# Optimization experiments

Measured on AMD Instinct MI355X. Metric: run time of the kernel, lower is better.

The kernel has to match this reference:

```python
import jax, jax.numpy as jnp
import numpy as np

N_NODES = 50000
N_EDGES = 1600000
D_IN = 128
D_OUT = 128
EPS = 0.001  # GINConv(eps=0.001) hard-coded in the module


def setup_inputs() -> dict:
    key = jax.random.key(0)
    k_x, k_e, k_w1, k_b1, k_w2, k_b2 = jax.random.split(key, 6)
    x = jax.random.normal(k_x, (N_NODES, D_IN), dtype=jnp.float32)
    edge_index = jax.random.randint(k_e, (2, N_EDGES), 0, N_NODES, dtype=jnp.int64)
    # MLP params (nn.Linear default init scale ~ 1/sqrt(fan_in))
    s1 = 1.0 / np.sqrt(D_IN)
    s2 = 1.0 / np.sqrt(D_OUT)
    W1 = jax.random.uniform(k_w1, (D_IN, D_OUT), jnp.float32, -s1, s1)
    b1 = jax.random.uniform(k_b1, (D_OUT,), jnp.float32, -s1, s1)
    W2 = jax.random.uniform(k_w2, (D_OUT, D_OUT), jnp.float32, -s2, s2)
    b2 = jax.random.uniform(k_b2, (D_OUT,), jnp.float32, -s2, s2)
    return {"x": x, "edge_index": edge_index, "W1": W1, "b1": b1, "W2": W2, "b2": b2}


def reference(x, edge_index, W1, b1, W2, b2):
    # GIN: out = MLP((1 + eps) * x + sum_{j in N(i)} x_j)
    src = edge_index[0]  # message source nodes
    dst = edge_index[1]  # aggregation targets
    agg = jax.ops.segment_sum(x[src], dst, num_segments=x.shape[0])  # [N, D_IN]
    h = (1.0 + EPS) * x + agg
    h = jax.nn.relu(h @ W1 + b1)
    return h @ W2 + b2
```

## Files before the change

### kernel.cpp

```cpp
#include <hip/hip_runtime.h>
#include <hip/hip_bf16.h>


#define N_NODES 50000
#define N_EDGES 1600000
#define D 128

#define NB_H 256
#define CHUNK (N_EDGES / NB_H)
#define EPT 7
#define BSH 6
#define BSZ 64
#define KB 782
#define CAPB 2560

typedef __attribute__((ext_vector_type(8))) short short8;
typedef __attribute__((ext_vector_type(4))) float float4v;

__device__ inline unsigned short f2b(float f) {
    unsigned u = __builtin_bit_cast(unsigned, f);
    u = u + 0x7fffu + ((u >> 16) & 1u);
    return (unsigned short)(u >> 16);
}
__device__ inline float b2f_lo(unsigned u) { return __builtin_bit_cast(float, u << 16); }
__device__ inline float b2f_hi(unsigned u) { return __builtin_bit_cast(float, u & 0xffff0000u); }

#define LPAD 136

__global__ __launch_bounds__(1024) void k_prep(const float* __restrict__ W1,
                                               const float* __restrict__ W2,
                                               unsigned short* __restrict__ Wt1,
                                               unsigned short* __restrict__ Wt2,
                                               unsigned* __restrict__ bpos,
                                               const int* __restrict__ ei,
                                               int* __restrict__ flag) {
    __shared__ int nz;
    if (threadIdx.x == 0) nz = 0;
    __syncthreads();
    if (blockIdx.x == 0 && threadIdx.x < 256 && ei[threadIdx.x * 2 + 1] != 0)
        atomicAdd(&nz, 1);
    __syncthreads();
    if (blockIdx.x == 0 && threadIdx.x == 0) *flag = (nz == 0) ? 1 : 0;
    if (blockIdx.x == 0)
        for (int i = threadIdx.x; i < KB; i += 1024) bpos[i] = 0u;

    const float* W = (blockIdx.x == 0) ? W1 : W2;
    unsigned short* Wt = (blockIdx.x == 0) ? Wt1 : Wt2;
    for (int i = threadIdx.x; i < 128 * 128; i += 1024) {
        int k = i >> 7;
        int n = i & 127;
        Wt[n * 128 + k] = f2b(W[k * 128 + n]);
    }
}

template <int AF32, int BIAS, int OUT_BF16>
__global__ __launch_bounds__(256, 2) void k_mm(const void* __restrict__ Av,
                                               const unsigned short* __restrict__ Wtg,
                                               const float* __restrict__ bias,
                                               void* __restrict__ outv, int M) {
    __shared__ short Al[128 * LPAD];
    __shared__ short Wt[128 * LPAD];
    __shared__ float bl[128];

    int t = threadIdx.x;
    int row0 = blockIdx.x * 128;

    if (AF32) {
        const float4* X4 = (const float4*)Av;
        #pragma unroll
        for (int i = 0; i < 16; ++i) {
            int idx = i * 256 + t;
            int r = idx >> 5;
            int c = idx & 31;
            float4 v = make_float4(0.f, 0.f, 0.f, 0.f);
            if (row0 + r < M) v = X4[(size_t)(row0 + r) * 32 + c];
            short4 o;
            o.x = (short)f2b(v.x); o.y = (short)f2b(v.y);
            o.z = (short)f2b(v.z); o.w = (short)f2b(v.w);
            *(short4*)&Al[r * LPAD + c * 4] = o;
        }
    } else {
        const uint4* A16 = (const uint4*)Av;
        #pragma unroll
        for (int i = 0; i < 8; ++i) {
            int idx = i * 256 + t;
            int r = idx >> 4;
            int c = idx & 15;
            uint4 v = make_uint4(0u, 0u, 0u, 0u);
            if (row0 + r < M) v = A16[(size_t)(row0 + r) * 16 + c];
            *(uint4*)&Al[r * LPAD + c * 8] = v;
        }
    }
    {
        const uint4* Wg4 = (const uint4*)Wtg;
        #pragma unroll
        for (int i = 0; i < 8; ++i) {
            int idx = i * 256 + t;
            int r = idx >> 4;
            int c = idx & 15;
            *(uint4*)&Wt[r * LPAD + c * 8] = Wg4[idx];
        }
    }
    if (BIAS && t < 32) ((float4*)bl)[t] = ((const float4*)bias)[t];
    __syncthreads();

    int wave = t >> 6;
    int lane = t & 63;
    int quad = lane >> 4;
    int l16 = lane & 15;
    int rowbase = wave * 32;

    float4v acc[2][8];
    #pragma unroll
    for (int mt = 0; mt < 2; ++mt)
        #pragma unroll
        for (int nt = 0; nt < 8; ++nt)
            acc[mt][nt] = (float4v){0.f, 0.f, 0.f, 0.f};

    #pragma unroll
    for (int kc = 0; kc < 4; ++kc) {
        int koff = kc * 32 + quad * 8;
        short8 a0 = *(const short8*)&Al[(rowbase + l16) * LPAD + koff];
        short8 a1 = *(const short8*)&Al[(rowbase + 16 + l16) * LPAD + koff];
        #pragma unroll
        for (int nt = 0; nt < 8; ++nt) {
            short8 bfr = *(const short8*)&Wt[(nt * 16 + l16) * LPAD + koff];
            acc[0][nt] = __builtin_amdgcn_mfma_f32_16x16x32_bf16(a0, bfr, acc[0][nt], 0, 0, 0);
            acc[1][nt] = __builtin_amdgcn_mfma_f32_16x16x32_bf16(a1, bfr, acc[1][nt], 0, 0, 0);
        }
    }

    #pragma unroll
    for (int mt = 0; mt < 2; ++mt) {
        int rloc = rowbase + mt * 16 + quad * 4;
        #pragma unroll
        for (int nt = 0; nt < 8; ++nt) {
            int col = nt * 16 + l16;
            float bv = BIAS ? bl[col] : 0.f;
            #pragma unroll
            for (int r = 0; r < 4; ++r) {
                int grow = row0 + rloc + r;
                if (grow < M) {
                    float v = acc[mt][nt][r] + bv;
                    if (OUT_BF16)
                        ((unsigned short*)outv)[(size_t)grow * 128 + col] = f2b(v);
                    else
                        ((float*)outv)[(size_t)grow * 128 + col] = v;
                }
            }
        }
    }
}

__global__ __launch_bounds__(1024) void k_sort(const int* __restrict__ ei,
                                               const int* __restrict__ flag,
                                               unsigned* __restrict__ bpos,
                                               unsigned* __restrict__ pairs) {
    __shared__ unsigned hist[KB];
    __shared__ unsigned bbase[KB];
    int b = blockIdx.x;
    int t = threadIdx.x;
    for (int i = t; i < KB; i += 1024) hist[i] = 0u;
    __syncthreads();
    int wide = *flag;
    int e0 = b * CHUNK;
    int dv[EPT], sv[EPT];
    #pragma unroll
    for (int i = 0; i < EPT; ++i) {
        dv[i] = -1; sv[i] = 0;
        int o = i * 1024 + t;
        if (o < CHUNK) {
            int e = e0 + o;
            long long di = (long long)N_EDGES + e;
            int d = wide ? ei[di * 2] : ei[di];
            int s = wide ? ei[(long long)e * 2] : ei[e];
            if ((unsigned)d < (unsigned)N_NODES) {
                dv[i] = d;
                sv[i] = ((unsigned)s < (unsigned)N_NODES) ? s : 0;
                atomicAdd(&hist[d >> BSH], 1u);
            }
        }
    }
    __syncthreads();
    for (int i = t; i < KB; i += 1024) {
        unsigned c = hist[i];
        bbase[i] = c ? atomicAdd(&bpos[i], c) : 0u;
        hist[i] = 0u;
    }
    __syncthreads();
    #pragma unroll
    for (int i = 0; i < EPT; ++i) {
        if (dv[i] >= 0) {
            int kb = dv[i] >> BSH;
            unsigned r = bbase[kb] + atomicAdd(&hist[kb], 1u);
            if (r < CAPB)
                pairs[(size_t)kb * CAPB + r] =
                    (unsigned)sv[i] | ((unsigned)(dv[i] & (BSZ - 1)) << 17);
        }
    }
}

__global__ __launch_bounds__(512) void k_bgather(const unsigned short* __restrict__ y,
                                                 const unsigned* __restrict__ pairs,
                                                 const unsigned* __restrict__ bpos,
                                                 const float* __restrict__ b1,
                                                 unsigned short* __restrict__ h) {
    __shared__ unsigned sbuf[CAPB];
    __shared__ int cnt[BSZ], loff[BSZ], pos[BSZ];
    int k = blockIdx.x;
    int t = threadIdx.x;
    if (t < BSZ) cnt[t] = 0;
    __syncthreads();
    int beg = k * CAPB;
    int tot = (int)bpos[k];
    if (tot > CAPB) tot = CAPB;
    for (int i = t; i < tot; i += 512)
        atomicAdd(&cnt[pairs[beg + i] >> 17], 1);
    __syncthreads();
    if (t < BSZ) {
        int v = cnt[t];
        int xs = v;
        #pragma unroll
        for (int off = 1; off < 64; off <<= 1) {
            int u0 = __shfl_up(xs, off, 64);
            if (t >= off) xs += u0;
        }
        loff[t] = xs - v;
        pos[t] = xs - v;
    }
    __syncthreads();
    for (int i = t; i < tot; i += 512) {
        unsigned p = pairs[beg + i];
        int r = atomicAdd(&pos[p >> 17], 1);
        if (r < CAPB) sbuf[r] = p & 0x1FFFFu;
    }
    __syncthreads();

    int w = t >> 6;
    int lane = t & 63;
    int g = lane >> 5;
    int u = lane & 31;
    const uint2* yr = (const uint2*)y;

    #pragma unroll 1
    for (int q = 0; q < 8; ++q) {
        int dl = w * 8 + q;
        int node = (k << BSH) + dl;
        if (node >= N_NODES) break;
        int jb = loff[dl];
        int je = jb + cnt[dl];
        if (je > CAPB) je = CAPB;
        float a0 = 0.f, a1 = 0.f, a2 = 0.f, a3 = 0.f;
        int j = jb + g;
        for (; j + 14 < je; j += 16) {
            int ss[8];
            #pragma unroll
            for (int q2 = 0; q2 < 8; ++q2) ss[q2] = (int)sbuf[j + 2 * q2];
            #pragma unroll
            for (int q2 = 0; q2 < 8; ++q2) {
                uint2 A = yr[(size_t)ss[q2] * 32 + u];
                a0 += b2f_lo(A.x); a1 += b2f_hi(A.x);
                a2 += b2f_lo(A.y); a3 += b2f_hi(A.y);
            }
        }
        for (; j < je; j += 2) {
            uint2 A = yr[(size_t)sbuf[j] * 32 + u];
            a0 += b2f_lo(A.x); a1 += b2f_hi(A.x);
            a2 += b2f_lo(A.y); a3 += b2f_hi(A.y);
        }
        a0 += __shfl_xor(a0, 32, 64); a1 += __shfl_xor(a1, 32, 64);
        a2 += __shfl_xor(a2, 32, 64); a3 += __shfl_xor(a3, 32, 64);
        if (g == 0) {
            uint2 S = yr[(size_t)node * 32 + u];
            float4 bv = ((const float4*)b1)[u];
            float f0 = fmaf(1.001f, b2f_lo(S.x), a0) + bv.x;
            float f1 = fmaf(1.001f, b2f_hi(S.x), a1) + bv.y;
            float f2 = fmaf(1.001f, b2f_lo(S.y), a2) + bv.z;
            float f3 = fmaf(1.001f, b2f_hi(S.y), a3) + bv.w;
            f0 = fmaxf(f0, 0.f); f1 = fmaxf(f1, 0.f);
            f2 = fmaxf(f2, 0.f); f3 = fmaxf(f3, 0.f);
            uint2 o;
            o.x = (unsigned)f2b(f0) | ((unsigned)f2b(f1) << 16);
            o.y = (unsigned)f2b(f2) | ((unsigned)f2b(f3) << 16);
            ((uint2*)h)[(size_t)node * 32 + u] = o;
        }
    }
}

extern "C" void kernel_launch(void* const* d_in, const int* in_sizes, int n_in,
                              void* d_out, int out_size, void* d_ws, size_t ws_size,
                              hipStream_t stream) {
    const float* x  = (const float*)d_in[0];
    const int*   ei = (const int*)d_in[1];
    const float* W1 = (const float*)d_in[2];
    const float* b1 = (const float*)d_in[3];
    const float* W2 = (const float*)d_in[4];
    const float* b2 = (const float*)d_in[5];
    float* out = (float*)d_out;

    char* ws = (char*)d_ws;
    unsigned short* y       = (unsigned short*)(ws);
    unsigned short* hb      = (unsigned short*)(ws + 12800000);
    unsigned*       pairs   = (unsigned*)(ws + 25600000);
    unsigned*       bpos    = (unsigned*)(ws + 33800000);
    unsigned short* Wt1     = (unsigned short*)(ws + 33900000);
    unsigned short* Wt2     = (unsigned short*)(ws + 34000000);
    int*            flag    = (int*)    (ws + 34100000);

    int gblocks = (N_NODES + 127) / 128;

    k_prep<<<2, 1024, 0, stream>>>(W1, W2, Wt1, Wt2, bpos, ei, flag);
    k_mm<1, 0, 1><<<gblocks, 256, 0, stream>>>(x, Wt1, nullptr, y, N_NODES);
    k_sort<<<NB_H, 1024, 0, stream>>>(ei, flag, bpos, pairs);
    k_bgather<<<KB, 512, 0, stream>>>(y, pairs, bpos, b1, hb);
    k_mm<0, 1, 0><<<gblocks, 256, 0, stream>>>(hb, Wt2, b2, out, N_NODES);
}
```

Measured before the change: 196.8 us.

## Fuse second GEMM into gather kernel and vectorize edge sort loads

```diff
diff --git a/kernel.cpp b/kernel.cpp
--- a/kernel.cpp
+++ b/kernel.cpp
@@ -6,13 +6,13 @@
 #define N_EDGES 1600000
 #define D 128
 
-#define NB_H 256
-#define CHUNK (N_EDGES / NB_H)
-#define EPT 7
+#define SB 196
+#define SCH 8192
 #define BSH 6
 #define BSZ 64
 #define KB 782
 #define CAPB 2560
+#define HP 136
 
 typedef __attribute__((ext_vector_type(8))) short short8;
 typedef __attribute__((ext_vector_type(4))) float float4v;
@@ -34,62 +34,47 @@
                                                unsigned* __restrict__ bpos,
                                                const int* __restrict__ ei,
                                                int* __restrict__ flag) {
-    __shared__ int nz;
-    if (threadIdx.x == 0) nz = 0;
-    __syncthreads();
-    if (blockIdx.x == 0 && threadIdx.x < 256 && ei[threadIdx.x * 2 + 1] != 0)
-        atomicAdd(&nz, 1);
-    __syncthreads();
-    if (blockIdx.x == 0 && threadIdx.x == 0) *flag = (nz == 0) ? 1 : 0;
-    if (blockIdx.x == 0)
+    int bb = blockIdx.x;
+    if (bb == 0) {
+        __shared__ int nz;
+        if (threadIdx.x == 0) nz = 0;
+        __syncthreads();
+        if (threadIdx.x < 256 && ei[threadIdx.x * 2 + 1] != 0) atomicAdd(&nz, 1);
+        __syncthreads();
+        if (threadIdx.x == 0) *flag = (nz == 0) ? 1 : 0;
         for (int i = threadIdx.x; i < KB; i += 1024) bpos[i] = 0u;
-
-    const float* W = (blockIdx.x == 0) ? W1 : W2;
-    unsigned short* Wt = (blockIdx.x == 0) ? Wt1 : Wt2;
-    for (int i = threadIdx.x; i < 128 * 128; i += 1024) {
+    }
+    const float* W = (bb < 4) ? W1 : W2;
+    unsigned short* Wt = (bb < 4) ? Wt1 : Wt2;
+    int q = bb & 3;
+    for (int i = q * 4096 + threadIdx.x; i < (q + 1) * 4096; i += 1024) {
         int k = i >> 7;
         int n = i & 127;
         Wt[n * 128 + k] = f2b(W[k * 128 + n]);
     }
 }
 
-template <int AF32, int BIAS, int OUT_BF16>
-__global__ __launch_bounds__(256, 2) void k_mm(const void* __restrict__ Av,
+__global__ __launch_bounds__(256, 2) void k_mm(const float* __restrict__ Av,
                                                const unsigned short* __restrict__ Wtg,
-                                               const float* __restrict__ bias,
-                                               void* __restrict__ outv, int M) {
+                                               unsigned short* __restrict__ y, int M) {
     __shared__ short Al[128 * LPAD];
     __shared__ short Wt[128 * LPAD];
-    __shared__ float bl[128];
 
     int t = threadIdx.x;
     int row0 = blockIdx.x * 128;
 
-    if (AF32) {
-        const float4* X4 = (const float4*)Av;
-        #pragma unroll
-        for (int i = 0; i < 16; ++i) {
-            int idx = i * 256 + t;
-            int r = idx >> 5;
-            int c = idx & 31;
-            float4 v = make_float4(0.f, 0.f, 0.f, 0.f);
-            if (row0 + r < M) v = X4[(size_t)(row0 + r) * 32 + c];
-            short4 o;
-            o.x = (short)f2b(v.x); o.y = (short)f2b(v.y);
-            o.z = (short)f2b(v.z); o.w = (short)f2b(v.w);
-            *(short4*)&Al[r * LPAD + c * 4] = o;
-        }
-    } else {
-        const uint4* A16 = (const uint4*)Av;
-        #pragma unroll
-        for (int i = 0; i < 8; ++i) {
-            int idx = i * 256 + t;
-            int r = idx >> 4;
-            int c = idx & 15;
-            uint4 v = make_uint4(0u, 0u, 0u, 0u);
-            if (row0 + r < M) v = A16[(size_t)(row0 + r) * 16 + c];
-            *(uint4*)&Al[r * LPAD + c * 8] = v;
-        }
+    const float4* X4 = (const float4*)Av;
+    #pragma unroll
+    for (int i = 0; i < 16; ++i) {
+        int idx = i * 256 + t;
+        int r = idx >> 5;
+        int c = idx & 31;
+        float4 v = make_float4(0.f, 0.f, 0.f, 0.f);
+        if (row0 + r < M) v = X4[(size_t)(row0 + r) * 32 + c];
+        short4 o;
+        o.x = (short)f2b(v.x); o.y = (short)f2b(v.y);
+        o.z = (short)f2b(v.z); o.w = (short)f2b(v.w);
+        *(short4*)&Al[r * LPAD + c * 4] = o;
     }
     {
         const uint4* Wg4 = (const uint4*)Wtg;
@@ -101,7 +86,6 @@
             *(uint4*)&Wt[r * LPAD + c * 8] = Wg4[idx];
         }
     }
-    if (BIAS && t < 32) ((float4*)bl)[t] = ((const float4*)bias)[t];
     __syncthreads();
 
     int wave = t >> 6;
@@ -136,17 +120,11 @@
         #pragma unroll
         for (int nt = 0; nt < 8; ++nt) {
             int col = nt * 16 + l16;
-            float bv = BIAS ? bl[col] : 0.f;
             #pragma unroll
             for (int r = 0; r < 4; ++r) {
                 int grow = row0 + rloc + r;
-                if (grow < M) {
-                    float v = acc[mt][nt][r] + bv;
-                    if (OUT_BF16)
-                        ((unsigned short*)outv)[(size_t)grow * 128 + col] = f2b(v);
-                    else
-                        ((float*)outv)[(size_t)grow * 128 + col] = v;
-                }
+                if (grow < M)
+                    y[(size_t)grow * 128 + col] = f2b(acc[mt][nt][r]);
             }
         }
     }
@@ -157,42 +135,57 @@
                                                unsigned* __restrict__ bpos,
                                                unsigned* __restrict__ pairs) {
     __shared__ unsigned hist[KB];
-    __shared__ unsigned bbase[KB];
     int b = blockIdx.x;
     int t = threadIdx.x;
     for (int i = t; i < KB; i += 1024) hist[i] = 0u;
     __syncthreads();
     int wide = *flag;
-    int e0 = b * CHUNK;
-    int dv[EPT], sv[EPT];
-    #pragma unroll
-    for (int i = 0; i < EPT; ++i) {
-        dv[i] = -1; sv[i] = 0;
-        int o = i * 1024 + t;
-        if (o < CHUNK) {
-            int e = e0 + o;
-            long long di = (long long)N_EDGES + e;
-            int d = wide ? ei[di * 2] : ei[di];
-            int s = wide ? ei[(long long)e * 2] : ei[e];
-            if ((unsigned)d < (unsigned)N_NODES) {
-                dv[i] = d;
-                sv[i] = ((unsigned)s < (unsigned)N_NODES) ? s : 0;
-                atomicAdd(&hist[d >> BSH], 1u);
-            }
-        }
+    int e0 = b * SCH + t * 8;
+    int dv[8], sv[8], rv[8];
+    if (e0 < N_EDGES) {
+        if (wide) {
+            const uint4* pd = (const uint4*)&ei[((size_t)N_EDGES + e0) * 2];
+            const uint4* ps = (const uint4*)&ei[(size_t)e0 * 2];
+            #pragma unroll
+            for (int j = 0; j < 4; ++j) {
+                uint4 qd = pd[j], qs = ps[j];
+                dv[2 * j] = (int)qd.x; dv[2 * j + 1] = (int)qd.z;
+                sv[2 * j] = (int)qs.x; sv[2 * j + 1] = (int)qs.z;
+            }
+        } else {
+            const uint4* pd = (const uint4*)&ei[(size_t)N_EDGES + e0];
+            const uint4* ps = (const uint4*)&ei[e0];
+            #pragma unroll
+            for (int j = 0; j < 2; ++j) {
+                uint4 qd = pd[j], qs = ps[j];
+                dv[4 * j] = (int)qd.x; dv[4 * j + 1] = (int)qd.y;
+                dv[4 * j + 2] = (int)qd.z; dv[4 * j + 3] = (int)qd.w;
+                sv[4 * j] = (int)qs.x; sv[4 * j + 1] = (int)qs.y;
+                sv[4 * j + 2] = (int)qs.z; sv[4 * j + 3] = (int)qs.w;
+            }
+        }
+    } else {
+        #pragma unroll
+        for (int i = 0; i < 8; ++i) dv[i] = -1;
+    }
+    #pragma unroll
+    for (int i = 0; i < 8; ++i) {
+        if ((unsigned)dv[i] < (unsigned)N_NODES) {
+            rv[i] = (int)atomicAdd(&hist[dv[i] >> BSH], 1u);
+            if ((unsigned)sv[i] >= (unsigned)N_NODES) sv[i] = 0;
+        } else dv[i] = -1;
     }
     __syncthreads();
     for (int i = t; i < KB; i += 1024) {
         unsigned c = hist[i];
-        bbase[i] = c ? atomicAdd(&bpos[i], c) : 0u;
-        hist[i] = 0u;
-    }
-    __syncthreads();
-    #pragma unroll
-    for (int i = 0; i < EPT; ++i) {
+        hist[i] = c ? atomicAdd(&bpos[i], c) : 0u;
+    }
+    __syncthreads();
+    #pragma unroll
+    for (int i = 0; i < 8; ++i) {
         if (dv[i] >= 0) {
             int kb = dv[i] >> BSH;
-            unsigned r = bbase[kb] + atomicAdd(&hist[kb], 1u);
+            unsigned r = hist[kb] + (unsigned)rv[i];
             if (r < CAPB)
                 pairs[(size_t)kb * CAPB + r] =
                     (unsigned)sv[i] | ((unsigned)(dv[i] & (BSZ - 1)) << 17);
@@ -204,8 +197,11 @@
                                                  const unsigned* __restrict__ pairs,
                                                  const unsigned* __restrict__ bpos,
                                                  const float* __restrict__ b1,
-                                                 unsigned short* __restrict__ h) {
+                                                 const unsigned short* __restrict__ Wt2g,
+                                                 const float* __restrict__ b2,
+                                                 float* __restrict__ out) {
     __shared__ unsigned sbuf[CAPB];
+    __shared__ short htile[BSZ * HP];
     __shared__ int cnt[BSZ], loff[BSZ], pos[BSZ];
     int k = blockIdx.x;
     int t = threadIdx.x;
@@ -232,7 +228,7 @@
     for (int i = t; i < tot; i += 512) {
         unsigned p = pairs[beg + i];
         int r = atomicAdd(&pos[p >> 17], 1);
-        if (r < CAPB) sbuf[r] = p & 0x1FFFFu;
+        sbuf[r] = p & 0x1FFFFu;
     }
     __syncthreads();
 
@@ -246,10 +242,8 @@
     for (int q = 0; q < 8; ++q) {
         int dl = w * 8 + q;
         int node = (k << BSH) + dl;
-        if (node >= N_NODES) break;
         int jb = loff[dl];
         int je = jb + cnt[dl];
-        if (je > CAPB) je = CAPB;
         float a0 = 0.f, a1 = 0.f, a2 = 0.f, a3 = 0.f;
         int j = jb + g;
         for (; j + 14 < je; j += 16) {
@@ -271,18 +265,52 @@
         a0 += __shfl_xor(a0, 32, 64); a1 += __shfl_xor(a1, 32, 64);
         a2 += __shfl_xor(a2, 32, 64); a3 += __shfl_xor(a3, 32, 64);
         if (g == 0) {
-            uint2 S = yr[(size_t)node * 32 + u];
-            float4 bv = ((const float4*)b1)[u];
-            float f0 = fmaf(1.001f, b2f_lo(S.x), a0) + bv.x;
-            float f1 = fmaf(1.001f, b2f_hi(S.x), a1) + bv.y;
-            float f2 = fmaf(1.001f, b2f_lo(S.y), a2) + bv.z;
-            float f3 = fmaf(1.001f, b2f_hi(S.y), a3) + bv.w;
-            f0 = fmaxf(f0, 0.f); f1 = fmaxf(f1, 0.f);
-            f2 = fmaxf(f2, 0.f); f3 = fmaxf(f3, 0.f);
-            uint2 o;
-            o.x = (unsigned)f2b(f0) | ((unsigned)f2b(f1) << 16);
-            o.y = (unsigned)f2b(f2) | ((unsigned)f2b(f3) << 16);
-            ((uint2*)h)[(size_t)node * 32 + u] = o;
+            uint2 o = make_uint2(0u, 0u);
+            if (node < N_NODES) {
+                uint2 S = yr[(size_t)node * 32 + u];
+                float4 bv = ((const float4*)b1)[u];
+                float f0 = fmaf(1.001f, b2f_lo(S.x), a0) + bv.x;
+                float f1 = fmaf(1.001f, b2f_hi(S.x), a1) + bv.y;
+                float f2 = fmaf(1.001f, b2f_lo(S.y), a2) + bv.z;
+                float f3 = fmaf(1.001f, b2f_hi(S.y), a3) + bv.w;
+                f0 = fmaxf(f0, 0.f); f1 = fmaxf(f1, 0.f);
+                f2 = fmaxf(f2, 0.f); f3 = fmaxf(f3, 0.f);
+                o.x = (unsigned)f2b(f0) | ((unsigned)f2b(f1) << 16);
+                o.y = (unsigned)f2b(f2) | ((unsigned)f2b(f3) << 16);
+            }
+            *(uint2*)&htile[dl * HP + u * 4] = o;
+        }
+    }
+    __syncthreads();
+
+    int quad = lane >> 4;
+    int l16 = lane & 15;
+    int mt = w >> 1;
+    int nh = w & 1;
+    float4v accB[4];
+    #pragma unroll
+    for (int nt2 = 0; nt2 < 4; ++nt2) accB[nt2] = (float4v){0.f, 0.f, 0.f, 0.f};
+    #pragma unroll
+    for (int kc = 0; kc < 4; ++kc) {
+        int koff = kc * 32 + quad * 8;
+        short8 a = *(const short8*)&htile[(mt * 16 + l16) * HP + koff];
+        #pragma unroll
+        for (int nt2 = 0; nt2 < 4; ++nt2) {
+            int col = nh * 64 + nt2 * 16 + l16;
+            short8 bfr = *(const short8*)&Wt2g[col * 128 + koff];
+            accB[nt2] = __builtin_amdgcn_mfma_f32_16x16x32_bf16(a, bfr, accB[nt2], 0, 0, 0);
+        }
+    }
+    int node0 = k << BSH;
+    #pragma unroll
+    for (int nt2 = 0; nt2 < 4; ++nt2) {
+        int col = nh * 64 + nt2 * 16 + l16;
+        float bb = b2[col];
+        #pragma unroll
+        for (int r = 0; r < 4; ++r) {
+            int grow = node0 + mt * 16 + quad * 4 + r;
+            if (grow < N_NODES)
+                out[(size_t)grow * 128 + col] = accB[nt2][r] + bb;
         }
     }
 }
@@ -300,18 +328,16 @@
 
     char* ws = (char*)d_ws;
     unsigned short* y       = (unsigned short*)(ws);
-    unsigned short* hb      = (unsigned short*)(ws + 12800000);
-    unsigned*       pairs   = (unsigned*)(ws + 25600000);
-    unsigned*       bpos    = (unsigned*)(ws + 33800000);
-    unsigned short* Wt1     = (unsigned short*)(ws + 33900000);
-    unsigned short* Wt2     = (unsigned short*)(ws + 34000000);
-    int*            flag    = (int*)    (ws + 34100000);
+    unsigned*       pairs   = (unsigned*)(ws + 12800000);
+    unsigned*       bpos    = (unsigned*)(ws + 21000000);
+    unsigned short* Wt1     = (unsigned short*)(ws + 21100000);
+    unsigned short* Wt2     = (unsigned short*)(ws + 21200000);
+    int*            flag    = (int*)    (ws + 21300000);
 
     int gblocks = (N_NODES + 127) / 128;
 
-    k_prep<<<2, 1024, 0, stream>>>(W1, W2, Wt1, Wt2, bpos, ei, flag);
-    k_mm<1, 0, 1><<<gblocks, 256, 0, stream>>>(x, Wt1, nullptr, y, N_NODES);
-    k_sort<<<NB_H, 1024, 0, stream>>>(ei, flag, bpos, pairs);
-    k_bgather<<<KB, 512, 0, stream>>>(y, pairs, bpos, b1, hb);
-    k_mm<0, 1, 0><<<gblocks, 256, 0, stream>>>(hb, Wt2, b2, out, N_NODES);
-}
+    k_prep<<<8, 1024, 0, stream>>>(W1, W2, Wt1, Wt2, bpos, ei, flag);
+    k_mm<<<gblocks, 256, 0, stream>>>(x, Wt1, y, N_NODES);
+    k_sort<<<SB, 1024, 0, stream>>>(ei, flag, bpos, pairs);
+    k_bgather<<<KB, 512, 0, stream>>>(y, pairs, bpos, b1, Wt2, b2, out);
+}
```

Result: no change. 194.2 us (-1.3%).
